# Kernel tuning notes

Measured on AMD Instinct MI355X. Metric: run time of the kernel, lower is better.

Reference implementation:

```python
import jax, jax.numpy as jnp
import numpy as np

N, E, D_IN, D_H, D_OUT, L = 100000, 300000, 128, 128, 3, 12


def _gconv(x, edges, W0, b0, W1, b1):
    # pytorch3d GraphConv: w0(x) + gather_scatter(w1(x), edges)
    y = x @ W0.T + b0                      # [N, D_out] self transform
    n = x @ W1.T + b1                      # [N, D_out] neighbor transform
    # undirected: each edge (i, j) adds n[j] to out[i] and n[i] to out[j]
    agg = jnp.zeros_like(y)
    agg = agg.at[edges[:, 0]].add(n[edges[:, 1]])
    agg = agg.at[edges[:, 1]].add(n[edges[:, 0]])
    return y + agg


def setup_inputs() -> dict:
    key = jax.random.key(0)
    ks = jax.random.split(key, 20)

    def lin(k, out_d, in_d):
        s = 1.0 / np.sqrt(in_d)
        return jax.random.uniform(k, (out_d, in_d), jnp.float32, -s, s)

    def bias(k, out_d, in_d):
        s = 1.0 / np.sqrt(in_d)
        return jax.random.uniform(k, (out_d,), jnp.float32, -s, s)

    features = jax.random.normal(ks[0], (N, D_IN), jnp.float32)
    edges = jax.random.randint(ks[1], (E, 2), 0, N, dtype=jnp.int32)

    # first layer (in -> hidden)
    W0_1, b0_1 = lin(ks[2], D_H, D_IN), bias(ks[3], D_H, D_IN)
    W1_1, b1_1 = lin(ks[4], D_H, D_IN), bias(ks[5], D_H, D_IN)
    # 12 hidden layers (hidden -> hidden), stacked for lax.scan
    W0_h = jax.vmap(lambda k: lin(k, D_H, D_H))(jax.random.split(ks[6], L))
    b0_h = jax.vmap(lambda k: bias(k, D_H, D_H))(jax.random.split(ks[7], L))
    W1_h = jax.vmap(lambda k: lin(k, D_H, D_H))(jax.random.split(ks[8], L))
    b1_h = jax.vmap(lambda k: bias(k, D_H, D_H))(jax.random.split(ks[9], L))
    # last layer (hidden -> out)
    W0_l, b0_l = lin(ks[10], D_OUT, D_H), bias(ks[11], D_OUT, D_H)
    W1_l, b1_l = lin(ks[12], D_OUT, D_H), bias(ks[13], D_OUT, D_H)

    return {
        "features": features, "edges": edges,
        "W0_1": W0_1, "b0_1": b0_1, "W1_1": W1_1, "b1_1": b1_1,
        "W0_h": W0_h, "b0_h": b0_h, "W1_h": W1_h, "b1_h": b1_h,
        "W0_l": W0_l, "b0_l": b0_l, "W1_l": W1_l, "b1_l": b1_l,
    }


def reference(features, edges, W0_1, b0_1, W1_1, b1_1,
              W0_h, b0_h, W1_h, b1_h, W0_l, b0_l, W1_l, b1_l):
    x = jax.nn.relu(_gconv(features, edges, W0_1, b0_1, W1_1, b1_1))
    residual = x

    def step(x, p):
        W0, b0, W1, b1 = p
        return jax.nn.relu(_gconv(x, edges, W0, b0, W1, b1)), None

    x, _ = jax.lax.scan(step, x, (W0_h, b0_h, W1_h, b1_h))
    auxiliary = x
    vertices = _gconv(residual + x, edges, W0_l, b0_l, W1_l, b1_l)
    return vertices, auxiliary
```

## Files before the change

kernel.cpp:

```cpp
#include <hip/hip_runtime.h>
#include <hip/hip_bf16.h>

#define D 128
#define OSTR 136

typedef float f32x4  __attribute__((ext_vector_type(4)));
typedef __attribute__((ext_vector_type(8))) __bf16 bh8;

union UV { uint4 u; bh8 h; };

__device__ inline float bf2f(unsigned short u) {
    union { unsigned int i; float f; } x; x.i = ((unsigned int)u) << 16; return x.f;
}
__device__ inline unsigned short f2bf(float f) {
    union { float f; unsigned int i; } x; x.f = f;
    return (unsigned short)((x.i + 0x7fffu + ((x.i >> 16) & 1u)) >> 16);
}
__device__ inline void acc2(unsigned int u, float& a, float& b) {
    union { unsigned int i; float f; } lo, hi;
    lo.i = u << 16; hi.i = u & 0xffff0000u;
    a += lo.f; b += hi.f;
}
__device__ inline unsigned int addb2(unsigned int ua, unsigned int ub) {
    union { unsigned int i; float f; } la, ha, lb, hb;
    la.i = ua << 16; ha.i = ua & 0xffff0000u;
    lb.i = ub << 16; hb.i = ub & 0xffff0000u;
    return ((unsigned int)f2bf(ha.f + hb.f) << 16) | f2bf(la.f + lb.f);
}

__global__ void k_hist(const int* __restrict__ edges, int E, int* __restrict__ deg) {
    int e = blockIdx.x * blockDim.x + threadIdx.x;
    if (e < E) {
        atomicAdd(&deg[edges[2 * e]], 1);
        atomicAdd(&deg[edges[2 * e + 1]], 1);
    }
}

__global__ void k_scan1(const int* __restrict__ deg, int n,
                        int* __restrict__ incl, int* __restrict__ bsum) {
    __shared__ int lds[1024];
    int t = threadIdx.x;
    int i = blockIdx.x * 1024 + t;
    int v = (i < n) ? deg[i] : 0;
    int cur = v;
    lds[t] = cur;
    __syncthreads();
    for (int off = 1; off < 1024; off <<= 1) {
        int add = (t >= off) ? lds[t - off] : 0;
        __syncthreads();
        cur += add;
        lds[t] = cur;
        __syncthreads();
    }
    if (i < n) incl[i] = cur;
    if (t == 1023) bsum[blockIdx.x] = cur;
}

__global__ void k_scan2(int* __restrict__ bsum, int nb) {
    __shared__ int lds[128];
    int t = threadIdx.x;
    int v = (t < nb) ? bsum[t] : 0;
    int cur = v;
    lds[t] = cur;
    __syncthreads();
    for (int off = 1; off < 128; off <<= 1) {
        int add = (t >= off) ? lds[t - off] : 0;
        __syncthreads();
        cur += add;
        lds[t] = cur;
        __syncthreads();
    }
    if (t < nb) bsum[t] = cur - v;
}

__global__ void k_scan3(const int* __restrict__ incl, const int* __restrict__ deg,
                        const int* __restrict__ bsum, int n, int twoE,
                        int* __restrict__ rowstart, int* __restrict__ cursor) {
    int i = blockIdx.x * blockDim.x + threadIdx.x;
    if (i < n) {
        int r = incl[i] - deg[i] + bsum[i >> 10];
        rowstart[i] = r;
        cursor[i] = r;
    }
    if (i == 0) rowstart[n] = twoE;
}

__global__ void k_fill(const int* __restrict__ edges, int E,
                       int* __restrict__ cursor, int* __restrict__ adj) {
    int e = blockIdx.x * blockDim.x + threadIdx.x;
    if (e < E) {
        int a = edges[2 * e], b = edges[2 * e + 1];
        adj[atomicAdd(&cursor[a], 1)] = b;
        adj[atomicAdd(&cursor[b], 1)] = a;
    }
}

__global__ void k_wprep(const float* __restrict__ W0_1, const float* __restrict__ W1_1,
                        const float* __restrict__ W0_h, const float* __restrict__ W1_h,
                        unsigned short* __restrict__ wb) {
    int idx = blockIdx.x * 256 + threadIdx.x;
    if (idx >= 13 * 2 * 128 * 128) return;
    int k = idx & 127;
    int o = (idx >> 7) & 127;
    int m = (idx >> 14) & 1;
    int l = idx >> 15;
    const float* src = (l == 0) ? (m ? W1_1 : W0_1)
                                : ((m ? W1_h : W0_h) + (size_t)(l - 1) * 16384);
    float v = src[o * 128 + k];
    int kk = m * 128 + k;
    wb[(size_t)l * 32768 + (kk >> 5) * 4096 + o * 32 + (kk & 31)] = f2bf(v);
}

__global__ void k_cvt(const float* __restrict__ in, unsigned short* __restrict__ out, int n4) {
    int i = blockIdx.x * blockDim.x + threadIdx.x;
    if (i >= n4) return;
    f32x4 v = *(const f32x4*)&in[(size_t)i * 4];
    unsigned short u[4];
    #pragma unroll
    for (int j = 0; j < 4; ++j) u[j] = f2bf(v[j]);
    *(uint2*)&out[(size_t)i * 4] = *(uint2*)u;
}

__global__ __launch_bounds__(256) void k_agg(
    const unsigned short* __restrict__ x, const int* __restrict__ rowstart,
    const int* __restrict__ adj, unsigned short* __restrict__ s, int n) {
    int node = blockIdx.x * 4 + (threadIdx.x >> 6);
    int lane = threadIdx.x & 63;
    if (node >= n) return;
    int r0 = rowstart[node], r1 = rowstart[node + 1];
    float a[8], b[8];
    #pragma unroll
    for (int k = 0; k < 8; ++k) { a[k] = 0.f; b[k] = 0.f; }
    for (int p = r0; p < r1; p += 8) {
        int q = p + (lane & 7);
        int idx = (q < r1) ? adj[q] : 0;
        unsigned int u[8];
        #pragma unroll
        for (int k = 0; k < 8; ++k) {
            int j = __shfl(idx, k);
            u[k] = *(const unsigned int*)&x[(size_t)j * D + lane * 2];
        }
        #pragma unroll
        for (int k = 0; k < 8; ++k)
            if (p + k < r1) acc2(u[k], a[k], b[k]);
    }
    float f0 = ((a[0] + a[1]) + (a[2] + a[3])) + ((a[4] + a[5]) + (a[6] + a[7]));
    float f1 = ((b[0] + b[1]) + (b[2] + b[3])) + ((b[4] + b[5]) + (b[6] + b[7]));
    unsigned int out = ((unsigned int)f2bf(f1) << 16) | f2bf(f0);
    *(unsigned int*)&s[(size_t)node * D + lane * 2] = out;
}

__global__ __launch_bounds__(256) void k_gemm(
    const unsigned short* __restrict__ x,
    const unsigned short* __restrict__ s,
    const unsigned short* __restrict__ wb,
    const float* __restrict__ b0, const float* __restrict__ b1,
    const int* __restrict__ deg,
    unsigned short* __restrict__ out,
    float* __restrict__ out32,
    const unsigned short* __restrict__ resid,
    unsigned short* __restrict__ zout,
    int n, int do_relu) {
    __shared__ __align__(16) unsigned short LDS[128 * OSTR];
    int t = threadIdx.x;
    int node0 = blockIdx.x * 128;
    int lane = t & 63;
    int wave = t >> 6;
    int wm = (wave & 1) * 64;
    int wn = (wave >> 1) * 64;
    int mlane = lane & 15;
    int quad = lane >> 4;

    f32x4 acc[4][4];
    #pragma unroll
    for (int i = 0; i < 4; ++i)
        #pragma unroll
        for (int j = 0; j < 4; ++j) acc[i][j] = (f32x4){0.f, 0.f, 0.f, 0.f};

    #pragma unroll
    for (int kc = 0; kc < 8; ++kc) {
        const unsigned short* srcA = (kc < 4) ? x : s;
        int kbase = (kc & 3) * 32;
        bh8 af[4], bf_[4];
        #pragma unroll
        for (int i = 0; i < 4; ++i) {
            int g = node0 + wm + i * 16 + mlane;
            UV v; v.u = (uint4){0u, 0u, 0u, 0u};
            if (g < n) v.u = *(const uint4*)&srcA[(size_t)g * D + kbase + quad * 8];
            af[i] = v.h;
        }
        #pragma unroll
        for (int j = 0; j < 4; ++j)
            bf_[j] = *(const bh8*)&wb[(size_t)kc * 4096 + (wn + j * 16 + mlane) * 32 + quad * 8];
        #pragma unroll
        for (int i = 0; i < 4; ++i)
            #pragma unroll
            for (int j = 0; j < 4; ++j)
                acc[i][j] = __builtin_amdgcn_mfma_f32_16x16x32_bf16(af[i], bf_[j], acc[i][j], 0, 0, 0);
    }

    #pragma unroll
    for (int i = 0; i < 4; ++i) {
        int mrow = wm + i * 16 + quad * 4;
        #pragma unroll
        for (int j = 0; j < 4; ++j) {
            int nn = wn + j * 16 + mlane;
            float b0v = b0[nn], b1v = b1[nn];
            #pragma unroll
            for (int r = 0; r < 4; ++r) {
                int g = node0 + mrow + r;
                float dg = (g < n) ? (float)deg[g] : 0.f;
                float val = acc[i][j][r] + b0v + dg * b1v;
                if (do_relu) val = fmaxf(val, 0.f);
                LDS[(mrow + r) * OSTR + nn] = f2bf(val);
            }
        }
    }
    __syncthreads();
    #pragma unroll
    for (int pass = 0; pass < 8; ++pass) {
        int row = pass * 16 + (t >> 4);
        int seg = (t & 15) * 8;
        int g = node0 + row;
        if (g < n) {
            uint4 v = *(const uint4*)&LDS[row * OSTR + seg];
            *(uint4*)&out[(size_t)g * D + seg] = v;
            if (zout) {
                uint4 rr = *(const uint4*)&resid[(size_t)g * D + seg];
                uint4 zz;
                zz.x = addb2(v.x, rr.x);
                zz.y = addb2(v.y, rr.y);
                zz.z = addb2(v.z, rr.z);
                zz.w = addb2(v.w, rr.w);
                *(uint4*)&zout[(size_t)g * D + seg] = zz;
            }
        }
    }
    if (out32) {
        #pragma unroll
        for (int pass = 0; pass < 16; ++pass) {
            int row = pass * 8 + (t >> 5);
            int seg = (t & 31) * 4;
            int g = node0 + row;
            if (g < n) {
                f32x4 v;
                #pragma unroll
                for (int j = 0; j < 4; ++j) v[j] = bf2f(LDS[row * OSTR + seg + j]);
                *(f32x4*)&out32[(size_t)g * D + seg] = v;
            }
        }
    }
}

__global__ void k_last(const unsigned short* __restrict__ z, const unsigned short* __restrict__ sz,
                       const float* __restrict__ W0, const float* __restrict__ b0,
                       const float* __restrict__ W1, const float* __restrict__ b1,
                       const int* __restrict__ deg, float* __restrict__ vert, int n) {
    int t = threadIdx.x;
    int lane = t & 63;
    int node = blockIdx.x * 4 + (t >> 6);
    if (node >= n) return;
    float z0 = bf2f(z[(size_t)node * D + lane]), z1 = bf2f(z[(size_t)node * D + 64 + lane]);
    float s0 = bf2f(sz[(size_t)node * D + lane]), s1 = bf2f(sz[(size_t)node * D + 64 + lane]);
    float dg = (float)deg[node];
    #pragma unroll
    for (int o = 0; o < 3; ++o) {
        float p = z0 * W0[o * D + lane] + z1 * W0[o * D + 64 + lane]
                + s0 * W1[o * D + lane] + s1 * W1[o * D + 64 + lane];
        for (int off = 32; off > 0; off >>= 1) p += __shfl_down(p, off);
        if (lane == 0) vert[(size_t)node * 3 + o] = p + b0[o] + dg * b1[o];
    }
}

extern "C" void kernel_launch(void* const* d_in, const int* in_sizes, int n_in,
                              void* d_out, int out_size, void* d_ws, size_t ws_size,
                              hipStream_t stream) {
    const float* features = (const float*)d_in[0];
    const int*   edges    = (const int*)d_in[1];
    const float* W0_1 = (const float*)d_in[2];
    const float* b0_1 = (const float*)d_in[3];
    const float* W1_1 = (const float*)d_in[4];
    const float* b1_1 = (const float*)d_in[5];
    const float* W0_h = (const float*)d_in[6];
    const float* b0_h = (const float*)d_in[7];
    const float* W1_h = (const float*)d_in[8];
    const float* b1_h = (const float*)d_in[9];
    const float* W0_l = (const float*)d_in[10];
    const float* b0_l = (const float*)d_in[11];
    const float* W1_l = (const float*)d_in[12];
    const float* b1_l = (const float*)d_in[13];

    const int N_ = 100000, E_ = 300000;
    float* vert = (float*)d_out;
    float* aux  = (float*)d_out + (size_t)N_ * 3;

    char* w = (char*)d_ws;
    auto alloc = [&](size_t bytes) {
        char* p = w;
        w += (bytes + 255) & ~(size_t)255;
        return p;
    };
    unsigned short* wb    = (unsigned short*)alloc((size_t)13 * 32768 * 2);
    unsigned short* xf    = (unsigned short*)alloc((size_t)N_ * D * 2);
    unsigned short* resid = (unsigned short*)alloc((size_t)N_ * D * 2);
    unsigned short* xa    = (unsigned short*)alloc((size_t)N_ * D * 2);
    unsigned short* xb    = (unsigned short*)alloc((size_t)N_ * D * 2);
    unsigned short* sb    = (unsigned short*)alloc((size_t)N_ * D * 2);
    int* deg    = (int*)alloc((size_t)N_ * 4);
    int* incl   = (int*)alloc((size_t)N_ * 4);
    int* rowst  = (int*)alloc((size_t)(N_ + 1) * 4);
    int* cursor = (int*)alloc((size_t)N_ * 4);
    int* bsum   = (int*)alloc(128 * 4);
    int* adj    = (int*)alloc((size_t)2 * E_ * 4);

    hipMemsetAsync(deg, 0, (size_t)N_ * 4, stream);
    k_hist<<<(E_ + 255) / 256, 256, 0, stream>>>(edges, E_, deg);
    int nb = (N_ + 1023) / 1024;
    k_scan1<<<nb, 1024, 0, stream>>>(deg, N_, incl, bsum);
    k_scan2<<<1, 128, 0, stream>>>(bsum, nb);
    k_scan3<<<(N_ + 255) / 256, 256, 0, stream>>>(incl, deg, bsum, N_, 2 * E_, rowst, cursor);
    k_fill<<<(E_ + 255) / 256, 256, 0, stream>>>(edges, E_, cursor, adj);

    k_wprep<<<(13 * 2 * 16384 + 255) / 256, 256, 0, stream>>>(W0_1, W1_1, W0_h, W1_h, wb);
    k_cvt<<<(N_ * D / 4 + 255) / 256, 256, 0, stream>>>(features, xf, N_ * D / 4);

    int gblocks = (N_ + 127) / 128;
    int ablocks = (N_ + 3) / 4;

    k_agg<<<ablocks, 256, 0, stream>>>(xf, rowst, adj, sb, N_);
    k_gemm<<<gblocks, 256, 0, stream>>>(xf, sb, wb, b0_1, b1_1, deg, resid,
                                        nullptr, nullptr, nullptr, N_, 1);

    for (int h = 0; h < 12; ++h) {
        const unsigned short* in = (h == 0) ? resid : ((h & 1) ? xa : xb);
        unsigned short* outp = (h & 1) ? xb : xa;
        float* o32 = (h == 11) ? aux : nullptr;
        const unsigned short* radd = (h == 11) ? resid : nullptr;
        unsigned short* zo = (h == 11) ? xf : nullptr;
        k_agg<<<ablocks, 256, 0, stream>>>(in, rowst, adj, sb, N_);
        k_gemm<<<gblocks, 256, 0, stream>>>(in, sb, wb + (size_t)(1 + h) * 32768,
                                            b0_h + h * 128, b1_h + h * 128, deg,
                                            outp, o32, radd, zo, N_, 1);
    }

    k_agg<<<ablocks, 256, 0, stream>>>(xf, rowst, adj, sb, N_);
    k_last<<<ablocks, 256, 0, stream>>>(xf, sb, W0_l, b0_l, W1_l, b1_l, deg, vert, N_);
}
```

Baseline: 1.260 ms.

## Swizzle block-to-node mapping across XCD chunks, shrink GEMM tile, nontemporal stores

Remaps block indices so consecutive blocks (round-robined across the 8 XCDs) each cover a contiguous chunk of nodes, aiming for better L2 locality per XCD in the aggregation and GEMM kernels. The GEMM tile drops from 128 to 64 rows per block, which doubles the block count and halves LDS use. Output stores become nontemporal to avoid polluting cache. CHUNK*8 = 100352 is hardcoded to cover N, so correctness depends on N being no larger than that.

```diff
diff --git a/kernel.cpp b/kernel.cpp
--- a/kernel.cpp
+++ b/kernel.cpp
@@ -3,8 +3,10 @@
 
 #define D 128
 #define OSTR 136
+#define CHUNK 12544
 
 typedef float f32x4  __attribute__((ext_vector_type(4)));
+typedef unsigned int u32x4 __attribute__((ext_vector_type(4)));
 typedef __attribute__((ext_vector_type(8))) __bf16 bh8;
 
 union UV { uint4 u; bh8 h; };
@@ -124,7 +126,7 @@
 __global__ __launch_bounds__(256) void k_agg(
     const unsigned short* __restrict__ x, const int* __restrict__ rowstart,
     const int* __restrict__ adj, unsigned short* __restrict__ s, int n) {
-    int node = blockIdx.x * 4 + (threadIdx.x >> 6);
+    int node = (blockIdx.x & 7) * CHUNK + (blockIdx.x >> 3) * 4 + (threadIdx.x >> 6);
     int lane = threadIdx.x & 63;
     if (node >= n) return;
     int r0 = rowstart[node], r1 = rowstart[node + 1];
@@ -161,19 +163,20 @@
     const unsigned short* __restrict__ resid,
     unsigned short* __restrict__ zout,
     int n, int do_relu) {
-    __shared__ __align__(16) unsigned short LDS[128 * OSTR];
+    __shared__ __align__(16) unsigned short LDS[64 * OSTR];
+    int node0 = (blockIdx.x & 7) * CHUNK + (blockIdx.x >> 3) * 64;
+    if (node0 >= n) return;
     int t = threadIdx.x;
-    int node0 = blockIdx.x * 128;
     int lane = t & 63;
     int wave = t >> 6;
-    int wm = (wave & 1) * 64;
-    int wn = (wave >> 1) * 64;
+    int wm = (wave >> 1) * 32;
+    int wn = (wave & 1) * 64;
     int mlane = lane & 15;
     int quad = lane >> 4;
 
-    f32x4 acc[4][4];
-    #pragma unroll
-    for (int i = 0; i < 4; ++i)
+    f32x4 acc[2][4];
+    #pragma unroll
+    for (int i = 0; i < 2; ++i)
         #pragma unroll
         for (int j = 0; j < 4; ++j) acc[i][j] = (f32x4){0.f, 0.f, 0.f, 0.f};
 
@@ -181,9 +184,9 @@
     for (int kc = 0; kc < 8; ++kc) {
         const unsigned short* srcA = (kc < 4) ? x : s;
         int kbase = (kc & 3) * 32;
-        bh8 af[4], bf_[4];
-        #pragma unroll
-        for (int i = 0; i < 4; ++i) {
+        bh8 af[2], bf_[4];
+        #pragma unroll
+        for (int i = 0; i < 2; ++i) {
             int g = node0 + wm + i * 16 + mlane;
             UV v; v.u = (uint4){0u, 0u, 0u, 0u};
             if (g < n) v.u = *(const uint4*)&srcA[(size_t)g * D + kbase + quad * 8];
@@ -193,14 +196,14 @@
         for (int j = 0; j < 4; ++j)
             bf_[j] = *(const bh8*)&wb[(size_t)kc * 4096 + (wn + j * 16 + mlane) * 32 + quad * 8];
         #pragma unroll
-        for (int i = 0; i < 4; ++i)
+        for (int i = 0; i < 2; ++i)
             #pragma unroll
             for (int j = 0; j < 4; ++j)
                 acc[i][j] = __builtin_amdgcn_mfma_f32_16x16x32_bf16(af[i], bf_[j], acc[i][j], 0, 0, 0);
     }
 
     #pragma unroll
-    for (int i = 0; i < 4; ++i) {
+    for (int i = 0; i < 2; ++i) {
         int mrow = wm + i * 16 + quad * 4;
         #pragma unroll
         for (int j = 0; j < 4; ++j) {
@@ -218,27 +221,27 @@
     }
     __syncthreads();
     #pragma unroll
-    for (int pass = 0; pass < 8; ++pass) {
+    for (int pass = 0; pass < 4; ++pass) {
         int row = pass * 16 + (t >> 4);
         int seg = (t & 15) * 8;
         int g = node0 + row;
         if (g < n) {
-            uint4 v = *(const uint4*)&LDS[row * OSTR + seg];
-            *(uint4*)&out[(size_t)g * D + seg] = v;
+            u32x4 v = *(const u32x4*)&LDS[row * OSTR + seg];
+            __builtin_nontemporal_store(v, (u32x4*)&out[(size_t)g * D + seg]);
             if (zout) {
-                uint4 rr = *(const uint4*)&resid[(size_t)g * D + seg];
-                uint4 zz;
+                u32x4 rr = *(const u32x4*)&resid[(size_t)g * D + seg];
+                u32x4 zz;
                 zz.x = addb2(v.x, rr.x);
                 zz.y = addb2(v.y, rr.y);
                 zz.z = addb2(v.z, rr.z);
                 zz.w = addb2(v.w, rr.w);
-                *(uint4*)&zout[(size_t)g * D + seg] = zz;
+                __builtin_nontemporal_store(zz, (u32x4*)&zout[(size_t)g * D + seg]);
             }
         }
     }
     if (out32) {
         #pragma unroll
-        for (int pass = 0; pass < 16; ++pass) {
+        for (int pass = 0; pass < 8; ++pass) {
             int row = pass * 8 + (t >> 5);
             int seg = (t & 31) * 4;
             int g = node0 + row;
@@ -246,7 +249,7 @@
                 f32x4 v;
                 #pragma unroll
                 for (int j = 0; j < 4; ++j) v[j] = bf2f(LDS[row * OSTR + seg + j]);
-                *(f32x4*)&out32[(size_t)g * D + seg] = v;
+                __builtin_nontemporal_store(v, (f32x4*)&out32[(size_t)g * D + seg]);
             }
         }
     }
@@ -324,8 +327,9 @@
     k_wprep<<<(13 * 2 * 16384 + 255) / 256, 256, 0, stream>>>(W0_1, W1_1, W0_h, W1_h, wb);
     k_cvt<<<(N_ * D / 4 + 255) / 256, 256, 0, stream>>>(features, xf, N_ * D / 4);
 
-    int gblocks = (N_ + 127) / 128;
-    int ablocks = (N_ + 3) / 4;
+    int gblocks = 8 * ((CHUNK) / 64);
+    int ablocks = 8 * ((CHUNK) / 4);
+    int ablocks_plain = (N_ + 3) / 4;
 
     k_agg<<<ablocks, 256, 0, stream>>>(xf, rowst, adj, sb, N_);
     k_gemm<<<gblocks, 256, 0, stream>>>(xf, sb, wb, b0_1, b1_1, deg, resid,
@@ -344,5 +348,5 @@
     }
 
     k_agg<<<ablocks, 256, 0, stream>>>(xf, rowst, adj, sb, N_);
-    k_last<<<ablocks, 256, 0, stream>>>(xf, sb, W0_l, b0_l, W1_l, b1_l, deg, vert, N_);
-}
+    k_last<<<ablocks_plain, 256, 0, stream>>>(xf, sb, W0_l, b0_l, W1_l, b1_l, deg, vert, N_);
+}
```

Result: no change. 1.271 ms (+0.9%).
